# Performance work log

Measured on AMD Instinct MI355X. Metric: run time of the kernel, lower is better.

The kernel has to match this reference:

```python
import jax, jax.numpy as jnp
import numpy as np

MU = 1.0          # stability parameter
DT = 0.01         # Euler step
EPS = 1e-9        # matches E in the torch source
BOUND = float(np.pi / 2)  # hard_bounds = (-pi/2, pi/2)
N_NODES = 200_000
N_EDGES = 12_800_000  # avg degree 64


def setup_inputs() -> dict:
    key = jax.random.key(0)
    ks = jax.random.split(key, 9)
    n, ne = N_NODES, N_EDGES
    # distributions mirror the torch initialization
    x = jax.random.normal(ks[0], (n,), jnp.float32) * 0.1
    y = jax.random.normal(ks[1], (n,), jnp.float32) * 0.1
    w = (jax.random.uniform(ks[2], (n,), jnp.float32) * 2 - 1) * 4.0 + 2.0
    amplitudes = (jax.random.uniform(ks[3], (n,), jnp.float32) * 2 - 1) * 2.0 + 1.0
    phase = (jax.random.uniform(ks[4], (n,), jnp.float32) * 2 - 1) * np.pi
    ha = jax.random.normal(ks[5], (n,), jnp.float32) * 0.5
    b = jax.random.normal(ks[6], (n,), jnp.float32) * 0.1
    edge_src = jax.random.randint(ks[7], (ne,), 0, n, jnp.int32)
    edge_dst = jax.random.randint(ks[8], (ne,), 0, n, jnp.int32)
    return {"x": x, "y": y, "w": w, "amplitudes": amplitudes, "phase": phase,
            "ha": ha, "b": b, "edge_src": edge_src, "edge_dst": edge_dst}


def reference(x, y, w, amplitudes, phase, ha, b, edge_src, edge_dst):
    n = x.shape[0]
    # r^2 = x^2 + y^2 + E  (torch computes sqrt(..+E) then squares it)
    r2 = x * x + y * y + EPS
    dx = (MU - r2) * x - w * y
    dy = (MU - r2) * y + w * x
    # edge coupling: for edge (j=src -> i=dst):
    #   d*_i += ha_i * sin(theta_j - theta_i) * (*_j - *_i)
    theta = jnp.arctan2(y, x + EPS)                       # [n]
    coef = ha[edge_dst] * jnp.sin(theta[edge_src] - theta[edge_dst])  # [ne]
    cx = jax.ops.segment_sum(coef * (x[edge_src] - x[edge_dst]), edge_dst, num_segments=n)
    cy = jax.ops.segment_sum(coef * (y[edge_src] - y[edge_dst]), edge_dst, num_segments=n)
    # Euler step (x update is internal state; angles depend only on new y)
    y_new = y + (dy + cy) * DT
    x_new = x + (dx + cx) * DT
    angles = amplitudes * y_new + phase + b
    angles = jnp.clip(angles, -BOUND, BOUND)
    return angles
```

## Files before the change

kernel.cpp:

```cpp
#include <hip/hip_runtime.h>
#include <hip/hip_bf16.h>

#define MU_V    1.0f
#define DT_V    0.01f
#define EPS_V   1e-9f
#define BOUND_V 1.5707963267948966f

constexpr int NPB     = 1024;
constexpr int LOG_NPB = 10;
constexpr int NB_MAX  = 256;
constexpr int B1      = 512;
constexpr int EPT     = 16;
constexpr int EPB     = B1 * EPT;
constexpr int CAP     = 68608;
constexpr int RB      = 256;

__global__ void node_pre_kernel(const float* __restrict__ x_,
                                const float* __restrict__ y_,
                                const float* __restrict__ ha_,
                                float4* __restrict__ pack,
                                unsigned* __restrict__ zbuf,
                                int n, int nz) {
    int i = blockIdx.x * blockDim.x + threadIdx.x;
    if (i < nz) zbuf[i] = 0u;
    if (i >= n) return;
    float x = x_[i];
    float y = y_[i];
    float xe = x + EPS_V;
    float r2 = xe * xe + y * y;
    float s, c;
    if (r2 > 0.0f) {
        float rinv = rsqrtf(r2);
        s = y * rinv;
        c = xe * rinv;
    } else {
        s = 0.0f;
        c = 1.0f;
    }
    pack[i] = make_float4(s, c, y, ha_[i]);
}

__global__ __launch_bounds__(B1)
void bucket_scatter_kernel(const int* __restrict__ src,
                           const int* __restrict__ dst,
                           unsigned* __restrict__ cursors,
                           unsigned* __restrict__ buf,
                           int ne, int nb) {
    __shared__ unsigned cnt[NB_MAX];
    __shared__ unsigned gbase[NB_MAX];
    __shared__ unsigned loc[NB_MAX];
    int tid = threadIdx.x;
    for (int i = tid; i < nb; i += B1) cnt[i] = 0u;
    __syncthreads();
    long long base = (long long)blockIdx.x * EPB;

    if (base + EPB <= ne) {
        int4 rs4[EPT / 4], rd4[EPT / 4];
        #pragma unroll
        for (int it = 0; it < EPT / 4; ++it) {
            long long e = base + ((long long)(it * B1 + tid)) * 4;
            rs4[it] = *(const int4*)(src + e);
            rd4[it] = *(const int4*)(dst + e);
        }
        const int* sv = (const int*)rs4;
        const int* dv = (const int*)rd4;
        #pragma unroll
        for (int k = 0; k < EPT; ++k)
            atomicAdd(&cnt[((unsigned)dv[k]) >> LOG_NPB], 1u);
        __syncthreads();
        for (int b = tid; b < nb; b += B1) {
            unsigned c = cnt[b];
            gbase[b] = c ? atomicAdd(&cursors[b], c) : 0u;
            loc[b] = 0u;
        }
        __syncthreads();
        #pragma unroll
        for (int g = 0; g < EPT / 8; ++g) {
            unsigned pos[8], bb[8];
            #pragma unroll
            for (int j = 0; j < 8; ++j) {
                unsigned d = (unsigned)dv[g * 8 + j];
                bb[j] = d >> LOG_NPB;
                pos[j] = gbase[bb[j]] + atomicAdd(&loc[bb[j]], 1u);
            }
            #pragma unroll
            for (int j = 0; j < 8; ++j) {
                unsigned d = (unsigned)dv[g * 8 + j];
                unsigned s = (unsigned)sv[g * 8 + j];
                if (pos[j] < (unsigned)CAP)
                    buf[(size_t)bb[j] * CAP + pos[j]] = (s << LOG_NPB) | (d & (NPB - 1));
            }
        }
    } else {
        #pragma unroll
        for (int it = 0; it < EPT / 4; ++it) {
            long long e = base + ((long long)(it * B1 + tid)) * 4;
            if (e + 4 <= ne) {
                int4 d4 = *(const int4*)(dst + e);
                atomicAdd(&cnt[((unsigned)d4.x) >> LOG_NPB], 1u);
                atomicAdd(&cnt[((unsigned)d4.y) >> LOG_NPB], 1u);
                atomicAdd(&cnt[((unsigned)d4.z) >> LOG_NPB], 1u);
                atomicAdd(&cnt[((unsigned)d4.w) >> LOG_NPB], 1u);
            } else if (e < ne) {
                for (long long q = e; q < ne; ++q)
                    atomicAdd(&cnt[((unsigned)dst[q]) >> LOG_NPB], 1u);
            }
        }
        __syncthreads();
        for (int b = tid; b < nb; b += B1) {
            unsigned c = cnt[b];
            gbase[b] = c ? atomicAdd(&cursors[b], c) : 0u;
            loc[b] = 0u;
        }
        __syncthreads();
        #pragma unroll
        for (int it = 0; it < EPT / 4; ++it) {
            long long e = base + ((long long)(it * B1 + tid)) * 4;
            if (e + 4 <= ne) {
                int4 s4 = *(const int4*)(src + e);
                int4 d4 = *(const int4*)(dst + e);
                {
                    unsigned d = (unsigned)d4.x, s = (unsigned)s4.x, b = d >> LOG_NPB;
                    unsigned pos = gbase[b] + atomicAdd(&loc[b], 1u);
                    if (pos < (unsigned)CAP) buf[(size_t)b * CAP + pos] = (s << LOG_NPB) | (d & (NPB - 1));
                }
                {
                    unsigned d = (unsigned)d4.y, s = (unsigned)s4.y, b = d >> LOG_NPB;
                    unsigned pos = gbase[b] + atomicAdd(&loc[b], 1u);
                    if (pos < (unsigned)CAP) buf[(size_t)b * CAP + pos] = (s << LOG_NPB) | (d & (NPB - 1));
                }
                {
                    unsigned d = (unsigned)d4.z, s = (unsigned)s4.z, b = d >> LOG_NPB;
                    unsigned pos = gbase[b] + atomicAdd(&loc[b], 1u);
                    if (pos < (unsigned)CAP) buf[(size_t)b * CAP + pos] = (s << LOG_NPB) | (d & (NPB - 1));
                }
                {
                    unsigned d = (unsigned)d4.w, s = (unsigned)s4.w, b = d >> LOG_NPB;
                    unsigned pos = gbase[b] + atomicAdd(&loc[b], 1u);
                    if (pos < (unsigned)CAP) buf[(size_t)b * CAP + pos] = (s << LOG_NPB) | (d & (NPB - 1));
                }
            } else if (e < ne) {
                for (long long q = e; q < ne; ++q) {
                    unsigned d = (unsigned)dst[q], s = (unsigned)src[q], b = d >> LOG_NPB;
                    unsigned pos = gbase[b] + atomicAdd(&loc[b], 1u);
                    if (pos < (unsigned)CAP) buf[(size_t)b * CAP + pos] = (s << LOG_NPB) | (d & (NPB - 1));
                }
            }
        }
    }
}

__device__ __forceinline__ void reduce_entry(unsigned ent,
                                             const float4* __restrict__ pack,
                                             const float4* __restrict__ plocal,
                                             float* __restrict__ acc) {
    unsigned s  = ent >> LOG_NPB;
    unsigned dl = ent & (NPB - 1);
    float4 ps = pack[s];
    float4 pd = plocal[dl];
    float v = (pd.w * (ps.x * pd.y - ps.y * pd.x)) * (ps.z - pd.z);
    atomicAdd(&acc[dl], v);
}

__global__ __launch_bounds__(RB)
void bucket_reduce_kernel(const unsigned* __restrict__ cursors,
                          const unsigned* __restrict__ buf,
                          const float4* __restrict__ pack,
                          float* __restrict__ partial, int n, int nsub) {
    __shared__ float4 plocal[NPB];
    __shared__ float  acc[NPB];
    int b   = blockIdx.x / nsub;
    int sub = blockIdx.x % nsub;
    int tid = threadIdx.x;
    int node0 = b << LOG_NPB;
    for (int k = tid; k < NPB; k += RB) {
        int d = node0 + k;
        plocal[k] = (d < n) ? pack[d] : make_float4(0.f, 0.f, 0.f, 0.f);
        acc[k] = 0.0f;
    }
    __syncthreads();
    unsigned count = cursors[b];
    if (count > (unsigned)CAP) count = (unsigned)CAP;
    unsigned chunk = (((count + nsub - 1) / nsub) + 7u) & ~7u;
    unsigned lo = (unsigned)sub * chunk;
    unsigned hi = lo + chunk;
    if (hi > count) hi = count;
    unsigned span = (hi > lo) ? (hi - lo) : 0u;
    unsigned vend = lo + (span & ~7u);
    const unsigned* mybuf = buf + (size_t)b * CAP;
    for (unsigned i = lo + (unsigned)tid * 8u; i < vend; i += (unsigned)RB * 8u) {
        uint4 a4 = *(const uint4*)(mybuf + i);
        uint4 b4 = *(const uint4*)(mybuf + i + 4);
        reduce_entry(a4.x, pack, plocal, acc);
        reduce_entry(a4.y, pack, plocal, acc);
        reduce_entry(a4.z, pack, plocal, acc);
        reduce_entry(a4.w, pack, plocal, acc);
        reduce_entry(b4.x, pack, plocal, acc);
        reduce_entry(b4.y, pack, plocal, acc);
        reduce_entry(b4.z, pack, plocal, acc);
        reduce_entry(b4.w, pack, plocal, acc);
    }
    {
        unsigned idx = vend + (unsigned)tid;
        if (idx < hi)
            reduce_entry(mybuf[idx], pack, plocal, acc);
    }
    __syncthreads();
    float* myp = partial + ((size_t)b * nsub + sub) * NPB;
    for (int k = tid; k < NPB; k += RB) myp[k] = acc[k];
}

__device__ __forceinline__ void edge_one(int s, int d,
                                         const float4* __restrict__ pack,
                                         float* __restrict__ cy) {
    float4 ps = pack[s];
    float4 pd = pack[d];
    float v = (pd.w * (ps.x * pd.y - ps.y * pd.x)) * (ps.z - pd.z);
    atomicAdd(&cy[d], v);
}

__global__ void edge_kernel(const int* __restrict__ src,
                            const int* __restrict__ dst,
                            const float4* __restrict__ pack,
                            float* __restrict__ cy, int ne) {
    int t = blockIdx.x * blockDim.x + threadIdx.x;
    long long base = (long long)t * 4;
    if (base >= ne) return;
    if (base + 4 <= ne) {
        int4 s4 = *(const int4*)(src + base);
        int4 d4 = *(const int4*)(dst + base);
        edge_one(s4.x, d4.x, pack, cy);
        edge_one(s4.y, d4.y, pack, cy);
        edge_one(s4.z, d4.z, pack, cy);
        edge_one(s4.w, d4.w, pack, cy);
    } else {
        for (long long e = base; e < ne; ++e)
            edge_one(src[e], dst[e], pack, cy);
    }
}

__global__ void finalize_fast_kernel(const float* __restrict__ x_,
                                     const float* __restrict__ y_,
                                     const float* __restrict__ w_,
                                     const float* __restrict__ amp_,
                                     const float* __restrict__ ph_,
                                     const float* __restrict__ b_,
                                     const float* __restrict__ partial,
                                     float* __restrict__ out, int n, int nsub) {
    int i = blockIdx.x * blockDim.x + threadIdx.x;
    if (i >= n) return;
    int bk = i >> LOG_NPB;
    int dl = i & (NPB - 1);
    float cy = 0.0f;
    for (int s = 0; s < nsub; ++s)
        cy += partial[((size_t)bk * nsub + s) * NPB + dl];
    float x = x_[i];
    float y = y_[i];
    float w = w_[i];
    float r2 = x * x + y * y + EPS_V;
    float dy = (MU_V - r2) * y + w * x;
    float y_new = y + (dy + cy) * DT_V;
    float ang = amp_[i] * y_new + ph_[i] + b_[i];
    ang = fminf(fmaxf(ang, -BOUND_V), BOUND_V);
    out[i] = ang;
}

__global__ void finalize_kernel(const float* __restrict__ x_,
                                const float* __restrict__ y_,
                                const float* __restrict__ w_,
                                const float* __restrict__ amp_,
                                const float* __restrict__ ph_,
                                const float* __restrict__ b_,
                                const float* __restrict__ cy,
                                float* __restrict__ out, int n) {
    int i = blockIdx.x * blockDim.x + threadIdx.x;
    if (i >= n) return;
    float x = x_[i];
    float y = y_[i];
    float w = w_[i];
    float r2 = x * x + y * y + EPS_V;
    float dy = (MU_V - r2) * y + w * x;
    float y_new = y + (dy + cy[i]) * DT_V;
    float ang = amp_[i] * y_new + ph_[i] + b_[i];
    ang = fminf(fmaxf(ang, -BOUND_V), BOUND_V);
    out[i] = ang;
}

extern "C" void kernel_launch(void* const* d_in, const int* in_sizes, int n_in,
                              void* d_out, int out_size, void* d_ws, size_t ws_size,
                              hipStream_t stream) {
    const float* x_   = (const float*)d_in[0];
    const float* y_   = (const float*)d_in[1];
    const float* w_   = (const float*)d_in[2];
    const float* amp_ = (const float*)d_in[3];
    const float* ph_  = (const float*)d_in[4];
    const float* ha_  = (const float*)d_in[5];
    const float* b_   = (const float*)d_in[6];
    const int* edge_src = (const int*)d_in[7];
    const int* edge_dst = (const int*)d_in[8];
    float* out = (float*)d_out;

    int n  = in_sizes[0];
    int ne = in_sizes[7];
    int nb = (n + NPB - 1) >> LOG_NPB;

    auto align256 = [](size_t v) { return (v + 255) & ~(size_t)255; };
    size_t off_pack    = 0;
    size_t off_cursors = align256(off_pack + (size_t)n * 16);
    size_t off_partial = align256(off_cursors + (size_t)nb * 4);

    int nsub = 0;
    size_t off_buf = 0;
    for (int cand : {16, 12, 8, 4, 2, 1}) {
        size_t ob = align256(off_partial + (size_t)nb * cand * NPB * 4);
        if (ob + (size_t)nb * CAP * 4 <= ws_size) { nsub = cand; off_buf = ob; break; }
    }

    float4*   pack    = (float4*)((char*)d_ws + off_pack);
    unsigned* cursors = (unsigned*)((char*)d_ws + off_cursors);
    float*    cy      = (float*)((char*)d_ws + off_cursors);
    float*    partial = (float*)((char*)d_ws + off_partial);
    unsigned* buf     = (unsigned*)((char*)d_ws + off_buf);

    bool fast = (nsub > 0) && (nb <= NB_MAX) &&
                ((long long)n <= (1LL << (31 - LOG_NPB)));

    const int B = 256;
    if (fast) {
        node_pre_kernel<<<(n + B - 1) / B, B, 0, stream>>>(
            x_, y_, ha_, pack, cursors, n, nb);
        int blocks1 = (ne + EPB - 1) / EPB;
        bucket_scatter_kernel<<<blocks1, B1, 0, stream>>>(
            edge_src, edge_dst, cursors, buf, ne, nb);
        bucket_reduce_kernel<<<nb * nsub, RB, 0, stream>>>(
            cursors, buf, pack, partial, n, nsub);
        finalize_fast_kernel<<<(n + B - 1) / B, B, 0, stream>>>(
            x_, y_, w_, amp_, ph_, b_, partial, out, n, nsub);
    } else {
        node_pre_kernel<<<(n + B - 1) / B, B, 0, stream>>>(
            x_, y_, ha_, pack, (unsigned*)cy, n, n);
        int ngroups = (ne + 3) / 4;
        edge_kernel<<<(ngroups + B - 1) / B, B, 0, stream>>>(
            edge_src, edge_dst, pack, cy, ne);
        finalize_kernel<<<(n + B - 1) / B, B, 0, stream>>>(
            x_, y_, w_, amp_, ph_, b_, cy, out, n);
    }
}
```

Baseline: 283.1 us.

## Stage bucketed edges in LDS and write each bucket contiguously

The bucket scatter kernel now computes a block-local prefix scan over bucket counts, writes packed edges into a shared-memory staging array grouped by bucket, then has each wave copy whole bucket runs to global memory with consecutive lanes. This replaces scattered per-edge global stores with coalesced runs to cut write transactions. In exchange it adds 32KB of LDS per block, which may lower occupancy, plus extra barriers and a scan step. The new path applies only to full blocks; the tail path is unchanged.

```diff
diff --git a/kernel.cpp b/kernel.cpp
--- a/kernel.cpp
+++ b/kernel.cpp
@@ -14,6 +14,8 @@
 constexpr int EPB     = B1 * EPT;
 constexpr int CAP     = 68608;
 constexpr int RB      = 256;
+
+static_assert(NB_MAX == 256, "block scan below assumes NB_MAX == 256 (4 waves)");
 
 __global__ void node_pre_kernel(const float* __restrict__ x_,
                                 const float* __restrict__ y_,
@@ -48,9 +50,13 @@
                            int ne, int nb) {
     __shared__ unsigned cnt[NB_MAX];
     __shared__ unsigned gbase[NB_MAX];
+    __shared__ unsigned lofs[NB_MAX];
     __shared__ unsigned loc[NB_MAX];
+    __shared__ unsigned wsum[4];
+    __shared__ unsigned ents[EPB];
+
     int tid = threadIdx.x;
-    for (int i = tid; i < nb; i += B1) cnt[i] = 0u;
+    for (int i = tid; i < NB_MAX; i += B1) cnt[i] = 0u;
     __syncthreads();
     long long base = (long long)blockIdx.x * EPB;
 
@@ -68,27 +74,51 @@
         for (int k = 0; k < EPT; ++k)
             atomicAdd(&cnt[((unsigned)dv[k]) >> LOG_NPB], 1u);
         __syncthreads();
-        for (int b = tid; b < nb; b += B1) {
-            unsigned c = cnt[b];
-            gbase[b] = c ? atomicAdd(&cursors[b], c) : 0u;
-            loc[b] = 0u;
-        }
-        __syncthreads();
-        #pragma unroll
-        for (int g = 0; g < EPT / 8; ++g) {
-            unsigned pos[8], bb[8];
+
+        unsigned myc = 0u, incl = 0u;
+        if (tid < NB_MAX) {
+            myc = cnt[tid];
+            incl = myc;
             #pragma unroll
-            for (int j = 0; j < 8; ++j) {
-                unsigned d = (unsigned)dv[g * 8 + j];
-                bb[j] = d >> LOG_NPB;
-                pos[j] = gbase[bb[j]] + atomicAdd(&loc[bb[j]], 1u);
+            for (int d = 1; d < 64; d <<= 1) {
+                unsigned up = __shfl_up(incl, d);
+                if ((tid & 63) >= d) incl += up;
             }
+            if ((tid & 63) == 63) wsum[tid >> 6] = incl;
+        }
+        __syncthreads();
+        if (tid < NB_MAX) {
+            unsigned wp = 0u;
+            int w = tid >> 6;
             #pragma unroll
-            for (int j = 0; j < 8; ++j) {
-                unsigned d = (unsigned)dv[g * 8 + j];
-                unsigned s = (unsigned)sv[g * 8 + j];
-                if (pos[j] < (unsigned)CAP)
-                    buf[(size_t)bb[j] * CAP + pos[j]] = (s << LOG_NPB) | (d & (NPB - 1));
+            for (int k = 0; k < 3; ++k)
+                if (k < w) wp += wsum[k];
+            lofs[tid] = wp + incl - myc;
+            gbase[tid] = myc ? atomicAdd(&cursors[tid], myc) : 0u;
+            loc[tid] = 0u;
+        }
+        __syncthreads();
+
+        #pragma unroll
+        for (int k = 0; k < EPT; ++k) {
+            unsigned d = (unsigned)dv[k];
+            unsigned s = (unsigned)sv[k];
+            unsigned b = d >> LOG_NPB;
+            unsigned p = atomicAdd(&loc[b], 1u);
+            ents[lofs[b] + p] = (s << LOG_NPB) | (d & (NPB - 1));
+        }
+        __syncthreads();
+
+        int wave = tid >> 6;
+        int lane = tid & 63;
+        for (int b = wave; b < nb; b += (B1 / 64)) {
+            unsigned c  = cnt[b];
+            unsigned gb = gbase[b];
+            unsigned lo = lofs[b];
+            for (unsigned i = (unsigned)lane; i < c; i += 64u) {
+                unsigned p = gb + i;
+                if (p < (unsigned)CAP)
+                    buf[(size_t)b * CAP + p] = ents[lo + i];
             }
         }
     } else {
```

Result: faster. 259.2 us (-8.4%).
